# Performance work log

Hardware: AMD Instinct MI355X
Metric: run time of the kernel (lower is better)

The kernel has to match this reference:

```python
import jax, jax.numpy as jnp
import numpy as np

B, SQ, SK, DK, DV = 16, 2048, 2048, 64, 64


def setup_inputs() -> dict:
    key = jax.random.key(0)
    kq, kk, kv, km = jax.random.split(key, 4)
    Q = jax.random.normal(kq, (B, SQ, DK), dtype=jnp.float32)
    K = jax.random.normal(kk, (B, SK, DK), dtype=jnp.float32)
    V = jax.random.normal(kv, (B, SK, DV), dtype=jnp.float32)
    mask = jax.random.randint(km, (B, 1, SK), 0, 2, dtype=jnp.int32)
    return {"Q": Q, "K": K, "V": V, "mask": mask}


def reference(Q, K, V, mask):
    d = K.shape[-1]
    # scores: (B, SQ, SK) -- full attention matrix, as in the torch module
    attn = jnp.einsum("bqd,bkd->bqk", Q, K) / (d ** 0.5)
    masked = mask == 0  # (B, 1, SK), broadcasts over query dim
    attn = jnp.where(masked, jnp.float32(-1e9), attn)
    attn = jax.nn.softmax(attn, axis=-1)
    attn = jnp.where(masked, jnp.float32(0.0), attn)
    output = jnp.einsum("bqk,bkv->bqv", attn, V)
    return (output, attn)
```

## Files before the change

### kernel.cpp

```cpp
#include <hip/hip_runtime.h>

#define NB   16
#define SQL  2048
#define SKL  2048
#define DKL  64
#define DVL  64
#define NE   (NB * SQL * DKL)

typedef __attribute__((ext_vector_type(8))) short short8;
typedef __attribute__((ext_vector_type(4))) short s16x4;
typedef __attribute__((ext_vector_type(4))) float f32x4;
typedef __attribute__((ext_vector_type(4))) int   i32x4;
typedef __attribute__((ext_vector_type(4))) unsigned u32x4;

#define SCALE_LOG2E 0.1803368801111204f
#define EXP2F(x) __builtin_amdgcn_exp2f(x)
#define MFMA32(a,b,c) __builtin_amdgcn_mfma_f32_16x16x32_bf16((a),(b),(c),0,0,0)

__device__ __forceinline__ short f2bf(float x) {
    unsigned u = __builtin_bit_cast(unsigned, x);
    u = (u + 0x7fffu + ((u >> 16) & 1u)) >> 16;
    return (short)u;
}
__device__ __forceinline__ float bf2f(short s) {
    return __builtin_bit_cast(float, ((unsigned)(unsigned short)s) << 16);
}

__device__ __forceinline__ short8 pk8(f32x4 a, f32x4 b) {
    unsigned w0, w1, w2, w3;
    asm("v_cvt_pk_bf16_f32 %0, %1, %2" : "=v"(w0) : "v"(a[0]), "v"(a[1]));
    asm("v_cvt_pk_bf16_f32 %0, %1, %2" : "=v"(w1) : "v"(a[2]), "v"(a[3]));
    asm("v_cvt_pk_bf16_f32 %0, %1, %2" : "=v"(w2) : "v"(b[0]), "v"(b[1]));
    asm("v_cvt_pk_bf16_f32 %0, %1, %2" : "=v"(w3) : "v"(b[2]), "v"(b[3]));
    u32x4 t = {w0, w1, w2, w3};
    return __builtin_bit_cast(short8, t);
}

__global__ __launch_bounds__(256)
void prep(const float* __restrict__ Q, const float* __restrict__ K,
          short* __restrict__ ws)
{
    short* qhi = ws;
    short* qlo = ws + (size_t)NE;
    short* khi = ws + (size_t)2 * NE;
    short* klo = ws + (size_t)3 * NE;

    size_t i4 = ((size_t)blockIdx.x * 256 + threadIdx.x) * 4;
    if (i4 >= NE) return;

    f32x4 q = *(const f32x4*)(Q + i4);
    f32x4 k = *(const f32x4*)(K + i4);
    s16x4 qh, ql, kh, kl;
    #pragma unroll
    for (int j = 0; j < 4; j++) {
        qh[j] = f2bf(q[j]);  ql[j] = f2bf(q[j] - bf2f(qh[j]));
        kh[j] = f2bf(k[j]);  kl[j] = f2bf(k[j] - bf2f(kh[j]));
    }
    *(s16x4*)(qhi + i4) = qh;
    *(s16x4*)(qlo + i4) = ql;
    *(s16x4*)(khi + i4) = kh;
    *(s16x4*)(klo + i4) = kl;
}

__global__ __launch_bounds__(256)
void vtrans(const float* __restrict__ V, short* __restrict__ vt)
{
    __shared__ short st[64][72];
    const int b  = blockIdx.x >> 5;
    const int kt = blockIdx.x & 31;
    const int t  = threadIdx.x;

    const int kr = t >> 2;
    const int c0 = (t & 3) * 16;
    const float* vsrc = V + ((size_t)(b * SKL) + kt * 64 + kr) * DVL + c0;
    #pragma unroll
    for (int j = 0; j < 4; j++) {
        f32x4 x = *(const f32x4*)(vsrc + j * 4);
        #pragma unroll
        for (int i = 0; i < 4; i++) st[kr][c0 + j * 4 + i] = f2bf(x[i]);
    }
    __syncthreads();

    const int vr = t >> 2;
    const int cc = (t & 3) * 16;
    short* dst = vt + (size_t)b * DVL * SKL + (size_t)vr * SKL + kt * 64 + cc;
    short o[16];
    #pragma unroll
    for (int m = 0; m < 16; m++) {
        int kk = cc + m;
        int tb = kk >> 5;
        int w5 = kk & 31;
        int qd = w5 >> 3;
        int jj = w5 & 7;
        int kl = tb * 32 + qd * 4 + (jj & 3) + ((jj >> 2) << 4);
        o[m] = st[kl][vr];
    }
    *(short8*)(dst)     = *(short8*)(o);
    *(short8*)(dst + 8) = *(short8*)(o + 8);
}

__global__ __launch_bounds__(256, 4)
void attn_fwd(const short* __restrict__ ws, const int* __restrict__ mask,
              float* __restrict__ out, float* __restrict__ attn)
{
    __shared__ __align__(16) char smem[16384 + 256];
    f32x4* s_acc = (f32x4*)smem;
    float* s_red = (float*)(smem + 16384);

    const int tid  = threadIdx.x;
    const int w    = tid >> 6;
    const int lane = tid & 63;
    const int l15  = tid & 15;
    const int quad = (tid & 63) >> 4;

    const int bid = blockIdx.x;
    const int swz = (bid & 7) * ((NB * SQL / 16) >> 3) + (bid >> 3);
    const int b     = swz >> 7;
    const int qbase = (swz & 127) * 16;

    const int k0 = w * (SKL / 4);
    const int k1 = k0 + SKL / 4;

    const short* qhi = ws + (size_t)(b * SQL + qbase) * DKL;
    const short* qlo = qhi + (size_t)NE;
    const short* khi = ws + (size_t)2 * NE + (size_t)b * SKL * DKL;
    const short* klo = khi + (size_t)NE;
    const short* vtg = ws + (size_t)4 * NE + (size_t)b * DVL * SKL;
    const int*   mk  = mask + b * SKL;

    short8 qa0h = *(const short8*)(qhi + (size_t)l15 * DKL + quad * 8);
    short8 qa1h = *(const short8*)(qhi + (size_t)l15 * DKL + 32 + quad * 8);
    short8 qa0l = *(const short8*)(qlo + (size_t)l15 * DKL + quad * 8);
    short8 qa1l = *(const short8*)(qlo + (size_t)l15 * DKL + 32 + quad * 8);

    float lsum = 0.f;
    for (int kb = k0; kb < k1; kb += 32) {
        size_t o0 = (size_t)(kb + l15) * DKL + quad * 8;
        size_t o1 = o0 + (size_t)16 * DKL;
        short8 h0l = *(const short8*)(khi + o0);
        short8 h0h = *(const short8*)(khi + o0 + 32);
        short8 h1l = *(const short8*)(khi + o1);
        short8 h1h = *(const short8*)(khi + o1 + 32);
        short8 l0l = *(const short8*)(klo + o0);
        short8 l0h = *(const short8*)(klo + o0 + 32);
        short8 l1l = *(const short8*)(klo + o1);
        short8 l1h = *(const short8*)(klo + o1 + 32);
        i32x4 m0 = *(const i32x4*)(mk + kb + quad * 4);
        i32x4 m1 = *(const i32x4*)(mk + kb + 16 + quad * 4);

        f32x4 z = {0.f, 0.f, 0.f, 0.f};
        f32x4 sA0 = MFMA32(h0l, qa0h, z);
        sA0 = MFMA32(l0l, qa0h, sA0);
        sA0 = MFMA32(h0l, qa0l, sA0);
        f32x4 sB0 = MFMA32(h0h, qa1h, z);
        sB0 = MFMA32(l0h, qa1h, sB0);
        sB0 = MFMA32(h0h, qa1l, sB0);
        f32x4 sA1 = MFMA32(h1l, qa0h, z);
        sA1 = MFMA32(l1l, qa0h, sA1);
        sA1 = MFMA32(h1l, qa0l, sA1);
        f32x4 sB1 = MFMA32(h1h, qa1h, z);
        sB1 = MFMA32(l1h, qa1h, sB1);
        sB1 = MFMA32(h1h, qa1l, sB1);

        #pragma unroll
        for (int r = 0; r < 4; r++) {
            lsum += EXP2F(fmaf(sA0[r] + sB0[r], SCALE_LOG2E, m0[r] ? 0.f : -1e9f));
            lsum += EXP2F(fmaf(sA1[r] + sB1[r], SCALE_LOG2E, m1[r] ? 0.f : -1e9f));
        }
    }
    lsum += __shfl_xor(lsum, 16, 64);
    lsum += __shfl_xor(lsum, 32, 64);
    if (lane < 16) s_red[w * 16 + l15] = lsum;
    __syncthreads();
    const float tot  = s_red[l15] + s_red[16 + l15] + s_red[32 + l15] + s_red[48 + l15];
    const float lg2i = -__log2f(tot);

    f32x4 acc[4];
    #pragma unroll
    for (int vt = 0; vt < 4; vt++) { f32x4 z = {0.f,0.f,0.f,0.f}; acc[vt] = z; }

    for (int kb = k0; kb < k1; kb += 32) {
        const short* vrow = vtg + kb + quad * 8;
        short8 vv0 = *(const short8*)(vrow + (size_t)(0 * 16 + l15) * SKL);
        short8 vv1 = *(const short8*)(vrow + (size_t)(1 * 16 + l15) * SKL);
        short8 vv2 = *(const short8*)(vrow + (size_t)(2 * 16 + l15) * SKL);
        short8 vv3 = *(const short8*)(vrow + (size_t)(3 * 16 + l15) * SKL);
        i32x4 m0 = *(const i32x4*)(mk + kb + quad * 4);
        i32x4 m1 = *(const i32x4*)(mk + kb + 16 + quad * 4);

        size_t o0 = (size_t)(kb + l15) * DKL + quad * 8;
        size_t o1 = o0 + (size_t)16 * DKL;
        short8 h0l = *(const short8*)(khi + o0);
        short8 h0h = *(const short8*)(khi + o0 + 32);
        short8 h1l = *(const short8*)(khi + o1);
        short8 h1h = *(const short8*)(khi + o1 + 32);
        short8 l0l = *(const short8*)(klo + o0);
        short8 l0h = *(const short8*)(klo + o0 + 32);
        short8 l1l = *(const short8*)(klo + o1);
        short8 l1h = *(const short8*)(klo + o1 + 32);

        f32x4 z = {0.f, 0.f, 0.f, 0.f};
        f32x4 sA0 = MFMA32(h0l, qa0h, z);
        sA0 = MFMA32(l0l, qa0h, sA0);
        sA0 = MFMA32(h0l, qa0l, sA0);
        f32x4 sB0 = MFMA32(h0h, qa1h, z);
        sB0 = MFMA32(l0h, qa1h, sB0);
        sB0 = MFMA32(h0h, qa1l, sB0);
        f32x4 sA1 = MFMA32(h1l, qa0h, z);
        sA1 = MFMA32(l1l, qa0h, sA1);
        sA1 = MFMA32(h1l, qa0l, sA1);
        f32x4 sB1 = MFMA32(h1h, qa1h, z);
        sB1 = MFMA32(l1h, qa1h, sB1);
        sB1 = MFMA32(h1h, qa1l, sB1);

        f32x4 p0, p1;
        #pragma unroll
        for (int r = 0; r < 4; r++) {
            p0[r] = EXP2F(fmaf(sA0[r] + sB0[r], SCALE_LOG2E, m0[r] ? lg2i : -1e9f));
            p1[r] = EXP2F(fmaf(sA1[r] + sB1[r], SCALE_LOG2E, m1[r] ? lg2i : -1e9f));
        }

        float* arow = attn + (size_t)(b * SQL + qbase + l15) * SKL + kb + quad * 4;
        *(f32x4*)arow        = p0;
        *(f32x4*)(arow + 16) = p1;

        short8 pa = pk8(p0, p1);
        acc[0] = MFMA32(pa, vv0, acc[0]);
        acc[1] = MFMA32(pa, vv1, acc[1]);
        acc[2] = MFMA32(pa, vv2, acc[2]);
        acc[3] = MFMA32(pa, vv3, acc[3]);
    }

    #pragma unroll
    for (int vt = 0; vt < 4; vt++) s_acc[vt * 256 + w * 64 + lane] = acc[vt];
    __syncthreads();

    f32x4 t_ = s_acc[w * 256 + 0 * 64 + lane];
    #pragma unroll
    for (int wp = 1; wp < 4; wp++) {
        f32x4 u = s_acc[w * 256 + wp * 64 + lane];
        #pragma unroll
        for (int r = 0; r < 4; r++) t_[r] += u[r];
    }
    #pragma unroll
    for (int r = 0; r < 4; r++)
        out[(size_t)(b * SQL + qbase + quad * 4 + r) * DVL + w * 16 + l15] = t_[r];
}

extern "C" void kernel_launch(void* const* d_in, const int* in_sizes, int n_in,
                              void* d_out, int out_size, void* d_ws, size_t ws_size,
                              hipStream_t stream) {
    const float* Q    = (const float*)d_in[0];
    const float* K    = (const float*)d_in[1];
    const float* V    = (const float*)d_in[2];
    const int*   mask = (const int*)d_in[3];
    float* out  = (float*)d_out;
    float* attn = out + (size_t)NB * SQL * DVL;
    short* ws   = (short*)d_ws;

    prep<<<dim3(NE / (256 * 4)), dim3(256), 0, stream>>>(Q, K, ws);
    vtrans<<<dim3(NB * (SKL / 64)), dim3(256), 0, stream>>>(V, ws + (size_t)4 * NE);
    attn_fwd<<<dim3(NB * (SQL / 16)), dim3(256), 0, stream>>>(ws, mask, out, attn);
}
```

Measured before the change: 560.8 us.

## Fuse softmax passes into single pass with separate attn normalization kernel

The attention kernel now computes QK^T and exp once. It accumulates the row sum and P·V in the same loop and writes unnormalized probabilities, then divides the output by the row sum. A new kernel rescales each attention row by the reciprocal of its sum. The aim is to drop the second QK^T recompute and the extra K loads, at the cost of an extra read-modify-write of the 256MB attn matrix. It also double-buffers K/V register loads and lowers the occupancy hint to 2.

```diff
diff --git a/kernel.cpp b/kernel.cpp
--- a/kernel.cpp
+++ b/kernel.cpp
@@ -99,7 +99,61 @@
     *(short8*)(dst + 8) = *(short8*)(o + 8);
 }
 
-__global__ __launch_bounds__(256, 4)
+#define LOADK(P, kb) {                                                  \
+    size_t o0 = (size_t)((kb) + l15) * DKL + quad * 8;                  \
+    size_t o1 = o0 + (size_t)16 * DKL;                                  \
+    P##h0l = *(const short8*)(khi + o0);                                \
+    P##h0h = *(const short8*)(khi + o0 + 32);                           \
+    P##h1l = *(const short8*)(khi + o1);                                \
+    P##h1h = *(const short8*)(khi + o1 + 32);                           \
+    P##l0l = *(const short8*)(klo + o0);                                \
+    P##l0h = *(const short8*)(klo + o0 + 32);                           \
+    P##l1l = *(const short8*)(klo + o1);                                \
+    P##l1h = *(const short8*)(klo + o1 + 32);                           \
+}
+
+#define LOADV(kb) {                                                     \
+    const short* vrow = vtg + (kb) + quad * 8;                          \
+    Vv0 = *(const short8*)(vrow + (size_t)(0 * 16 + l15) * SKL);        \
+    Vv1 = *(const short8*)(vrow + (size_t)(1 * 16 + l15) * SKL);        \
+    Vv2 = *(const short8*)(vrow + (size_t)(2 * 16 + l15) * SKL);        \
+    Vv3 = *(const short8*)(vrow + (size_t)(3 * 16 + l15) * SKL);        \
+}
+
+#define STEP(P, kb) {                                                   \
+    i32x4 m0 = *(const i32x4*)(mk + (kb) + quad * 4);                   \
+    i32x4 m1 = *(const i32x4*)(mk + (kb) + 16 + quad * 4);              \
+    f32x4 z = {0.f, 0.f, 0.f, 0.f};                                     \
+    f32x4 sA0 = MFMA32(P##h0l, qa0h, z);                                \
+    sA0 = MFMA32(P##l0l, qa0h, sA0);                                    \
+    sA0 = MFMA32(P##h0l, qa0l, sA0);                                    \
+    f32x4 sB0 = MFMA32(P##h0h, qa1h, z);                                \
+    sB0 = MFMA32(P##l0h, qa1h, sB0);                                    \
+    sB0 = MFMA32(P##h0h, qa1l, sB0);                                    \
+    f32x4 sA1 = MFMA32(P##h1l, qa0h, z);                                \
+    sA1 = MFMA32(P##l1l, qa0h, sA1);                                    \
+    sA1 = MFMA32(P##h1l, qa0l, sA1);                                    \
+    f32x4 sB1 = MFMA32(P##h1h, qa1h, z);                                \
+    sB1 = MFMA32(P##l1h, qa1h, sB1);                                    \
+    sB1 = MFMA32(P##h1h, qa1l, sB1);                                    \
+    f32x4 p0, p1;                                                       \
+    _Pragma("unroll")                                                   \
+    for (int r = 0; r < 4; r++) {                                       \
+        p0[r] = EXP2F(fmaf(sA0[r] + sB0[r], SCALE_LOG2E, m0[r] ? 0.f : -1e9f)); \
+        p1[r] = EXP2F(fmaf(sA1[r] + sB1[r], SCALE_LOG2E, m1[r] ? 0.f : -1e9f)); \
+        lsum += p0[r] + p1[r];                                          \
+    }                                                                   \
+    short8 pa = pk8(p0, p1);                                            \
+    acc0 = MFMA32(pa, Vv0, acc0);                                       \
+    acc1 = MFMA32(pa, Vv1, acc1);                                       \
+    acc2 = MFMA32(pa, Vv2, acc2);                                       \
+    acc3 = MFMA32(pa, Vv3, acc3);                                       \
+    float* arow = attn + (size_t)(b * SQL + qbase + l15) * SKL + (kb) + quad * 4; \
+    *(f32x4*)arow        = p0;                                          \
+    *(f32x4*)(arow + 16) = p1;                                          \
+}
+
+__global__ __launch_bounds__(256, 2)
 void attn_fwd(const short* __restrict__ ws, const int* __restrict__ mask,
               float* __restrict__ out, float* __restrict__ attn)
 {
@@ -119,7 +173,6 @@
     const int qbase = (swz & 127) * 16;
 
     const int k0 = w * (SKL / 4);
-    const int k1 = k0 + SKL / 4;
 
     const short* qhi = ws + (size_t)(b * SQL + qbase) * DKL;
     const short* qlo = qhi + (size_t)NE;
@@ -133,106 +186,34 @@
     short8 qa0l = *(const short8*)(qlo + (size_t)l15 * DKL + quad * 8);
     short8 qa1l = *(const short8*)(qlo + (size_t)l15 * DKL + 32 + quad * 8);
 
+    f32x4 acc0 = {0.f,0.f,0.f,0.f}, acc1 = acc0, acc2 = acc0, acc3 = acc0;
     float lsum = 0.f;
-    for (int kb = k0; kb < k1; kb += 32) {
-        size_t o0 = (size_t)(kb + l15) * DKL + quad * 8;
-        size_t o1 = o0 + (size_t)16 * DKL;
-        short8 h0l = *(const short8*)(khi + o0);
-        short8 h0h = *(const short8*)(khi + o0 + 32);
-        short8 h1l = *(const short8*)(khi + o1);
-        short8 h1h = *(const short8*)(khi + o1 + 32);
-        short8 l0l = *(const short8*)(klo + o0);
-        short8 l0h = *(const short8*)(klo + o0 + 32);
-        short8 l1l = *(const short8*)(klo + o1);
-        short8 l1h = *(const short8*)(klo + o1 + 32);
-        i32x4 m0 = *(const i32x4*)(mk + kb + quad * 4);
-        i32x4 m1 = *(const i32x4*)(mk + kb + 16 + quad * 4);
-
-        f32x4 z = {0.f, 0.f, 0.f, 0.f};
-        f32x4 sA0 = MFMA32(h0l, qa0h, z);
-        sA0 = MFMA32(l0l, qa0h, sA0);
-        sA0 = MFMA32(h0l, qa0l, sA0);
-        f32x4 sB0 = MFMA32(h0h, qa1h, z);
-        sB0 = MFMA32(l0h, qa1h, sB0);
-        sB0 = MFMA32(h0h, qa1l, sB0);
-        f32x4 sA1 = MFMA32(h1l, qa0h, z);
-        sA1 = MFMA32(l1l, qa0h, sA1);
-        sA1 = MFMA32(h1l, qa0l, sA1);
-        f32x4 sB1 = MFMA32(h1h, qa1h, z);
-        sB1 = MFMA32(l1h, qa1h, sB1);
-        sB1 = MFMA32(h1h, qa1l, sB1);
-
-        #pragma unroll
-        for (int r = 0; r < 4; r++) {
-            lsum += EXP2F(fmaf(sA0[r] + sB0[r], SCALE_LOG2E, m0[r] ? 0.f : -1e9f));
-            lsum += EXP2F(fmaf(sA1[r] + sB1[r], SCALE_LOG2E, m1[r] ? 0.f : -1e9f));
-        }
-    }
+
+    short8 Ah0l, Ah0h, Ah1l, Ah1h, Al0l, Al0h, Al1l, Al1h;
+    short8 Bh0l, Bh0h, Bh1l, Bh1h, Bl0l, Bl0h, Bl1l, Bl1h;
+    short8 Vv0, Vv1, Vv2, Vv3;
+
+    LOADK(A, k0);
+    for (int it = 0; it < 8; ++it) {
+        const int kb0 = k0 + it * 64;
+        LOADV(kb0);
+        LOADK(B, kb0 + 32);
+        STEP(A, kb0);
+        LOADV(kb0 + 32);
+        const int kbn = (it < 7) ? kb0 + 64 : k0;
+        LOADK(A, kbn);
+        STEP(B, kb0 + 32);
+    }
+
     lsum += __shfl_xor(lsum, 16, 64);
     lsum += __shfl_xor(lsum, 32, 64);
     if (lane < 16) s_red[w * 16 + l15] = lsum;
     __syncthreads();
-    const float tot  = s_red[l15] + s_red[16 + l15] + s_red[32 + l15] + s_red[48 + l15];
-    const float lg2i = -__log2f(tot);
-
-    f32x4 acc[4];
-    #pragma unroll
-    for (int vt = 0; vt < 4; vt++) { f32x4 z = {0.f,0.f,0.f,0.f}; acc[vt] = z; }
-
-    for (int kb = k0; kb < k1; kb += 32) {
-        const short* vrow = vtg + kb + quad * 8;
-        short8 vv0 = *(const short8*)(vrow + (size_t)(0 * 16 + l15) * SKL);
-        short8 vv1 = *(const short8*)(vrow + (size_t)(1 * 16 + l15) * SKL);
-        short8 vv2 = *(const short8*)(vrow + (size_t)(2 * 16 + l15) * SKL);
-        short8 vv3 = *(const short8*)(vrow + (size_t)(3 * 16 + l15) * SKL);
-        i32x4 m0 = *(const i32x4*)(mk + kb + quad * 4);
-        i32x4 m1 = *(const i32x4*)(mk + kb + 16 + quad * 4);
-
-        size_t o0 = (size_t)(kb + l15) * DKL + quad * 8;
-        size_t o1 = o0 + (size_t)16 * DKL;
-        short8 h0l = *(const short8*)(khi + o0);
-        short8 h0h = *(const short8*)(khi + o0 + 32);
-        short8 h1l = *(const short8*)(khi + o1);
-        short8 h1h = *(const short8*)(khi + o1 + 32);
-        short8 l0l = *(const short8*)(klo + o0);
-        short8 l0h = *(const short8*)(klo + o0 + 32);
-        short8 l1l = *(const short8*)(klo + o1);
-        short8 l1h = *(const short8*)(klo + o1 + 32);
-
-        f32x4 z = {0.f, 0.f, 0.f, 0.f};
-        f32x4 sA0 = MFMA32(h0l, qa0h, z);
-        sA0 = MFMA32(l0l, qa0h, sA0);
-        sA0 = MFMA32(h0l, qa0l, sA0);
-        f32x4 sB0 = MFMA32(h0h, qa1h, z);
-        sB0 = MFMA32(l0h, qa1h, sB0);
-        sB0 = MFMA32(h0h, qa1l, sB0);
-        f32x4 sA1 = MFMA32(h1l, qa0h, z);
-        sA1 = MFMA32(l1l, qa0h, sA1);
-        sA1 = MFMA32(h1l, qa0l, sA1);
-        f32x4 sB1 = MFMA32(h1h, qa1h, z);
-        sB1 = MFMA32(l1h, qa1h, sB1);
-        sB1 = MFMA32(h1h, qa1l, sB1);
-
-        f32x4 p0, p1;
-        #pragma unroll
-        for (int r = 0; r < 4; r++) {
-            p0[r] = EXP2F(fmaf(sA0[r] + sB0[r], SCALE_LOG2E, m0[r] ? lg2i : -1e9f));
-            p1[r] = EXP2F(fmaf(sA1[r] + sB1[r], SCALE_LOG2E, m1[r] ? lg2i : -1e9f));
-        }
-
-        float* arow = attn + (size_t)(b * SQL + qbase + l15) * SKL + kb + quad * 4;
-        *(f32x4*)arow        = p0;
-        *(f32x4*)(arow + 16) = p1;
-
-        short8 pa = pk8(p0, p1);
-        acc[0] = MFMA32(pa, vv0, acc[0]);
-        acc[1] = MFMA32(pa, vv1, acc[1]);
-        acc[2] = MFMA32(pa, vv2, acc[2]);
-        acc[3] = MFMA32(pa, vv3, acc[3]);
-    }
-
-    #pragma unroll
-    for (int vt = 0; vt < 4; vt++) s_acc[vt * 256 + w * 64 + lane] = acc[vt];
+
+    s_acc[0 * 256 + w * 64 + lane] = acc0;
+    s_acc[1 * 256 + w * 64 + lane] = acc1;
+    s_acc[2 * 256 + w * 64 + lane] = acc2;
+    s_acc[3 * 256 + w * 64 + lane] = acc3;
     __syncthreads();
 
     f32x4 t_ = s_acc[w * 256 + 0 * 64 + lane];
@@ -243,8 +224,32 @@
         for (int r = 0; r < 4; r++) t_[r] += u[r];
     }
     #pragma unroll
-    for (int r = 0; r < 4; r++)
-        out[(size_t)(b * SQL + qbase + quad * 4 + r) * DVL + w * 16 + l15] = t_[r];
+    for (int r = 0; r < 4; r++) {
+        int rr = quad * 4 + r;
+        float tt = s_red[rr] + s_red[16 + rr] + s_red[32 + rr] + s_red[48 + rr];
+        out[(size_t)(b * SQL + qbase + rr) * DVL + w * 16 + l15] = t_[r] / tt;
+    }
+}
+
+__global__ __launch_bounds__(256)
+void norm(float* __restrict__ attn)
+{
+    __shared__ float sw[4];
+    const int row = blockIdx.x;
+    float* p = attn + (size_t)row * SKL + threadIdx.x * 8;
+    f32x4 x0 = *(const f32x4*)p;
+    f32x4 x1 = *(const f32x4*)(p + 4);
+    float s = (x0[0] + x0[1]) + (x0[2] + x0[3])
+            + (x1[0] + x1[1]) + (x1[2] + x1[3]);
+    #pragma unroll
+    for (int off = 1; off < 64; off <<= 1) s += __shfl_xor(s, off, 64);
+    if ((threadIdx.x & 63) == 0) sw[threadIdx.x >> 6] = s;
+    __syncthreads();
+    const float inv = 1.0f / ((sw[0] + sw[1]) + (sw[2] + sw[3]));
+    #pragma unroll
+    for (int r = 0; r < 4; r++) { x0[r] *= inv; x1[r] *= inv; }
+    *(f32x4*)p       = x0;
+    *(f32x4*)(p + 4) = x1;
 }
 
 extern "C" void kernel_launch(void* const* d_in, const int* in_sizes, int n_in,
@@ -261,4 +266,5 @@
     prep<<<dim3(NE / (256 * 4)), dim3(256), 0, stream>>>(Q, K, ws);
     vtrans<<<dim3(NB * (SKL / 64)), dim3(256), 0, stream>>>(V, ws + (size_t)4 * NE);
     attn_fwd<<<dim3(NB * (SQL / 16)), dim3(256), 0, stream>>>(ws, mask, out, attn);
-}
+    norm<<<dim3(NB * SQL), dim3(256), 0, stream>>>(attn);
+}
```

Measured after the change: 525.8 us. 6.2% less time.

## Replace two-pass softmax with single pass plus separate attn normalization kernel

Applied to the files above, without the earlier changes.

The attention kernel now computes QK^T once, writes unnormalized exp scores to attn, accumulates PV and row sums in the same loop, and divides the output by the row sum at the end. A new norm kernel rereads each attn row, sums it and rescales it. Each block also handles 32 query rows instead of 16 so K/V loads are shared across two row tiles. This drops the second QK^T recomputation and K reload, but adds a full extra read and write of the 256MB attn matrix and lowers occupancy. No max subtraction is used, so exp can overflow for large scores.

```diff
diff --git a/kernel.cpp b/kernel.cpp
--- a/kernel.cpp
+++ b/kernel.cpp
@@ -99,13 +99,13 @@
     *(short8*)(dst + 8) = *(short8*)(o + 8);
 }
 
-__global__ __launch_bounds__(256, 4)
+__global__ __launch_bounds__(256, 2)
 void attn_fwd(const short* __restrict__ ws, const int* __restrict__ mask,
               float* __restrict__ out, float* __restrict__ attn)
 {
-    __shared__ __align__(16) char smem[16384 + 256];
+    __shared__ __align__(16) char smem[32768 + 512];
     f32x4* s_acc = (f32x4*)smem;
-    float* s_red = (float*)(smem + 16384);
+    float* s_red = (float*)(smem + 32768);
 
     const int tid  = threadIdx.x;
     const int w    = tid >> 6;
@@ -114,12 +114,11 @@
     const int quad = (tid & 63) >> 4;
 
     const int bid = blockIdx.x;
-    const int swz = (bid & 7) * ((NB * SQL / 16) >> 3) + (bid >> 3);
-    const int b     = swz >> 7;
-    const int qbase = (swz & 127) * 16;
+    const int swz = (bid & 7) * 128 + (bid >> 3);
+    const int b     = swz >> 6;
+    const int qbase = (swz & 63) * 32;
 
     const int k0 = w * (SKL / 4);
-    const int k1 = k0 + SKL / 4;
 
     const short* qhi = ws + (size_t)(b * SQL + qbase) * DKL;
     const short* qlo = qhi + (size_t)NE;
@@ -132,9 +131,18 @@
     short8 qa1h = *(const short8*)(qhi + (size_t)l15 * DKL + 32 + quad * 8);
     short8 qa0l = *(const short8*)(qlo + (size_t)l15 * DKL + quad * 8);
     short8 qa1l = *(const short8*)(qlo + (size_t)l15 * DKL + 32 + quad * 8);
-
-    float lsum = 0.f;
-    for (int kb = k0; kb < k1; kb += 32) {
+    short8 qb0h = *(const short8*)(qhi + (size_t)(16 + l15) * DKL + quad * 8);
+    short8 qb1h = *(const short8*)(qhi + (size_t)(16 + l15) * DKL + 32 + quad * 8);
+    short8 qb0l = *(const short8*)(qlo + (size_t)(16 + l15) * DKL + quad * 8);
+    short8 qb1l = *(const short8*)(qlo + (size_t)(16 + l15) * DKL + 32 + quad * 8);
+
+    f32x4 acc00 = {0.f,0.f,0.f,0.f}, acc01 = acc00, acc02 = acc00, acc03 = acc00;
+    f32x4 acc10 = acc00, acc11 = acc00, acc12 = acc00, acc13 = acc00;
+    float lsum0 = 0.f, lsum1 = 0.f;
+
+    for (int it = 0; it < 16; ++it) {
+        const int kb = k0 + it * 32;
+
         size_t o0 = (size_t)(kb + l15) * DKL + quad * 8;
         size_t o1 = o0 + (size_t)16 * DKL;
         short8 h0l = *(const short8*)(khi + o0);
@@ -145,6 +153,11 @@
         short8 l0h = *(const short8*)(klo + o0 + 32);
         short8 l1l = *(const short8*)(klo + o1);
         short8 l1h = *(const short8*)(klo + o1 + 32);
+        const short* vrow = vtg + kb + quad * 8;
+        short8 vv0 = *(const short8*)(vrow + (size_t)(0 * 16 + l15) * SKL);
+        short8 vv1 = *(const short8*)(vrow + (size_t)(1 * 16 + l15) * SKL);
+        short8 vv2 = *(const short8*)(vrow + (size_t)(2 * 16 + l15) * SKL);
+        short8 vv3 = *(const short8*)(vrow + (size_t)(3 * 16 + l15) * SKL);
         i32x4 m0 = *(const i32x4*)(mk + kb + quad * 4);
         i32x4 m1 = *(const i32x4*)(mk + kb + 16 + quad * 4);
 
@@ -161,90 +174,112 @@
         f32x4 sB1 = MFMA32(h1h, qa1h, z);
         sB1 = MFMA32(l1h, qa1h, sB1);
         sB1 = MFMA32(h1h, qa1l, sB1);
-
+        f32x4 tA0 = MFMA32(h0l, qb0h, z);
+        tA0 = MFMA32(l0l, qb0h, tA0);
+        tA0 = MFMA32(h0l, qb0l, tA0);
+        f32x4 tB0 = MFMA32(h0h, qb1h, z);
+        tB0 = MFMA32(l0h, qb1h, tB0);
+        tB0 = MFMA32(h0h, qb1l, tB0);
+        f32x4 tA1 = MFMA32(h1l, qb0h, z);
+        tA1 = MFMA32(l1l, qb0h, tA1);
+        tA1 = MFMA32(h1l, qb0l, tA1);
+        f32x4 tB1 = MFMA32(h1h, qb1h, z);
+        tB1 = MFMA32(l1h, qb1h, tB1);
+        tB1 = MFMA32(h1h, qb1l, tB1);
+
+        f32x4 p0, p1, q0, q1;
         #pragma unroll
         for (int r = 0; r < 4; r++) {
-            lsum += EXP2F(fmaf(sA0[r] + sB0[r], SCALE_LOG2E, m0[r] ? 0.f : -1e9f));
-            lsum += EXP2F(fmaf(sA1[r] + sB1[r], SCALE_LOG2E, m1[r] ? 0.f : -1e9f));
+            float bias0 = m0[r] ? 0.f : -1e9f;
+            float bias1 = m1[r] ? 0.f : -1e9f;
+            p0[r] = EXP2F(fmaf(sA0[r] + sB0[r], SCALE_LOG2E, bias0));
+            p1[r] = EXP2F(fmaf(sA1[r] + sB1[r], SCALE_LOG2E, bias1));
+            q0[r] = EXP2F(fmaf(tA0[r] + tB0[r], SCALE_LOG2E, bias0));
+            q1[r] = EXP2F(fmaf(tA1[r] + tB1[r], SCALE_LOG2E, bias1));
+            lsum0 += p0[r] + p1[r];
+            lsum1 += q0[r] + q1[r];
         }
-    }
-    lsum += __shfl_xor(lsum, 16, 64);
-    lsum += __shfl_xor(lsum, 32, 64);
-    if (lane < 16) s_red[w * 16 + l15] = lsum;
+
+        float* a0 = attn + (size_t)(b * SQL + qbase + l15) * SKL + kb + quad * 4;
+        float* a1 = attn + (size_t)(b * SQL + qbase + 16 + l15) * SKL + kb + quad * 4;
+        *(f32x4*)a0        = p0;
+        *(f32x4*)(a0 + 16) = p1;
+        *(f32x4*)a1        = q0;
+        *(f32x4*)(a1 + 16) = q1;
+
+        short8 pa = pk8(p0, p1);
+        short8 pb = pk8(q0, q1);
+        acc00 = MFMA32(pa, vv0, acc00);
+        acc01 = MFMA32(pa, vv1, acc01);
+        acc02 = MFMA32(pa, vv2, acc02);
+        acc03 = MFMA32(pa, vv3, acc03);
+        acc10 = MFMA32(pb, vv0, acc10);
+        acc11 = MFMA32(pb, vv1, acc11);
+        acc12 = MFMA32(pb, vv2, acc12);
+        acc13 = MFMA32(pb, vv3, acc13);
+    }
+
+    lsum0 += __shfl_xor(lsum0, 16, 64);
+    lsum0 += __shfl_xor(lsum0, 32, 64);
+    lsum1 += __shfl_xor(lsum1, 16, 64);
+    lsum1 += __shfl_xor(lsum1, 32, 64);
+    if (lane < 16) {
+        s_red[w * 16 + l15]      = lsum0;
+        s_red[64 + w * 16 + l15] = lsum1;
+    }
+
+    s_acc[0 * 256 + w * 64 + lane] = acc00;
+    s_acc[1 * 256 + w * 64 + lane] = acc01;
+    s_acc[2 * 256 + w * 64 + lane] = acc02;
+    s_acc[3 * 256 + w * 64 + lane] = acc03;
+    s_acc[4 * 256 + w * 64 + lane] = acc10;
+    s_acc[5 * 256 + w * 64 + lane] = acc11;
+    s_acc[6 * 256 + w * 64 + lane] = acc12;
+    s_acc[7 * 256 + w * 64 + lane] = acc13;
     __syncthreads();
-    const float tot  = s_red[l15] + s_red[16 + l15] + s_red[32 + l15] + s_red[48 + l15];
-    const float lg2i = -__log2f(tot);
-
-    f32x4 acc[4];
-    #pragma unroll
-    for (int vt = 0; vt < 4; vt++) { f32x4 z = {0.f,0.f,0.f,0.f}; acc[vt] = z; }
-
-    for (int kb = k0; kb < k1; kb += 32) {
-        const short* vrow = vtg + kb + quad * 8;
-        short8 vv0 = *(const short8*)(vrow + (size_t)(0 * 16 + l15) * SKL);
-        short8 vv1 = *(const short8*)(vrow + (size_t)(1 * 16 + l15) * SKL);
-        short8 vv2 = *(const short8*)(vrow + (size_t)(2 * 16 + l15) * SKL);
-        short8 vv3 = *(const short8*)(vrow + (size_t)(3 * 16 + l15) * SKL);
-        i32x4 m0 = *(const i32x4*)(mk + kb + quad * 4);
-        i32x4 m1 = *(const i32x4*)(mk + kb + 16 + quad * 4);
-
-        size_t o0 = (size_t)(kb + l15) * DKL + quad * 8;
-        size_t o1 = o0 + (size_t)16 * DKL;
-        short8 h0l = *(const short8*)(khi + o0);
-        short8 h0h = *(const short8*)(khi + o0 + 32);
-        short8 h1l = *(const short8*)(khi + o1);
-        short8 h1h = *(const short8*)(khi + o1 + 32);
-        short8 l0l = *(const short8*)(klo + o0);
-        short8 l0h = *(const short8*)(klo + o0 + 32);
-        short8 l1l = *(const short8*)(klo + o1);
-        short8 l1h = *(const short8*)(klo + o1 + 32);
-
-        f32x4 z = {0.f, 0.f, 0.f, 0.f};
-        f32x4 sA0 = MFMA32(h0l, qa0h, z);
-        sA0 = MFMA32(l0l, qa0h, sA0);
-        sA0 = MFMA32(h0l, qa0l, sA0);
-        f32x4 sB0 = MFMA32(h0h, qa1h, z);
-        sB0 = MFMA32(l0h, qa1h, sB0);
-        sB0 = MFMA32(h0h, qa1l, sB0);
-        f32x4 sA1 = MFMA32(h1l, qa0h, z);
-        sA1 = MFMA32(l1l, qa0h, sA1);
-        sA1 = MFMA32(h1l, qa0l, sA1);
-        f32x4 sB1 = MFMA32(h1h, qa1h, z);
-        sB1 = MFMA32(l1h, qa1h, sB1);
-        sB1 = MFMA32(h1h, qa1l, sB1);
-
-        f32x4 p0, p1;
+
+    #pragma unroll
+    for (int c = 0; c < 2; c++) {
+        const int T  = w * 2 + c;
+        const int g  = T >> 2;
+        const int vt = T & 3;
+        f32x4 t_ = s_acc[T * 256 + 0 * 64 + lane];
+        #pragma unroll
+        for (int wp = 1; wp < 4; wp++) {
+            f32x4 u = s_acc[T * 256 + wp * 64 + lane];
+            #pragma unroll
+            for (int r = 0; r < 4; r++) t_[r] += u[r];
+        }
         #pragma unroll
         for (int r = 0; r < 4; r++) {
-            p0[r] = EXP2F(fmaf(sA0[r] + sB0[r], SCALE_LOG2E, m0[r] ? lg2i : -1e9f));
-            p1[r] = EXP2F(fmaf(sA1[r] + sB1[r], SCALE_LOG2E, m1[r] ? lg2i : -1e9f));
+            const int qr = quad * 4 + r;
+            float tt = s_red[g * 64 + qr]      + s_red[g * 64 + 16 + qr]
+                     + s_red[g * 64 + 32 + qr] + s_red[g * 64 + 48 + qr];
+            out[(size_t)(b * SQL + qbase + g * 16 + qr) * DVL + vt * 16 + l15] =
+                t_[r] / tt;
         }
-
-        float* arow = attn + (size_t)(b * SQL + qbase + l15) * SKL + kb + quad * 4;
-        *(f32x4*)arow        = p0;
-        *(f32x4*)(arow + 16) = p1;
-
-        short8 pa = pk8(p0, p1);
-        acc[0] = MFMA32(pa, vv0, acc[0]);
-        acc[1] = MFMA32(pa, vv1, acc[1]);
-        acc[2] = MFMA32(pa, vv2, acc[2]);
-        acc[3] = MFMA32(pa, vv3, acc[3]);
-    }
-
-    #pragma unroll
-    for (int vt = 0; vt < 4; vt++) s_acc[vt * 256 + w * 64 + lane] = acc[vt];
+    }
+}
+
+__global__ __launch_bounds__(256)
+void norm(float* __restrict__ attn)
+{
+    __shared__ float sw[4];
+    const int row = blockIdx.x;
+    float* p = attn + (size_t)row * SKL + threadIdx.x * 8;
+    f32x4 x0 = *(const f32x4*)p;
+    f32x4 x1 = *(const f32x4*)(p + 4);
+    float s = (x0[0] + x0[1]) + (x0[2] + x0[3])
+            + (x1[0] + x1[1]) + (x1[2] + x1[3]);
+    #pragma unroll
+    for (int off = 1; off < 64; off <<= 1) s += __shfl_xor(s, off, 64);
+    if ((threadIdx.x & 63) == 0) sw[threadIdx.x >> 6] = s;
     __syncthreads();
-
-    f32x4 t_ = s_acc[w * 256 + 0 * 64 + lane];
-    #pragma unroll
-    for (int wp = 1; wp < 4; wp++) {
-        f32x4 u = s_acc[w * 256 + wp * 64 + lane];
-        #pragma unroll
-        for (int r = 0; r < 4; r++) t_[r] += u[r];
-    }
-    #pragma unroll
-    for (int r = 0; r < 4; r++)
-        out[(size_t)(b * SQL + qbase + quad * 4 + r) * DVL + w * 16 + l15] = t_[r];
+    const float inv = 1.0f / ((sw[0] + sw[1]) + (sw[2] + sw[3]));
+    #pragma unroll
+    for (int r = 0; r < 4; r++) { x0[r] *= inv; x1[r] *= inv; }
+    *(f32x4*)p       = x0;
+    *(f32x4*)(p + 4) = x1;
 }
 
 extern "C" void kernel_launch(void* const* d_in, const int* in_sizes, int n_in,
@@ -260,5 +295,6 @@
 
     prep<<<dim3(NE / (256 * 4)), dim3(256), 0, stream>>>(Q, K, ws);
     vtrans<<<dim3(NB * (SKL / 64)), dim3(256), 0, stream>>>(V, ws + (size_t)4 * NE);
-    attn_fwd<<<dim3(NB * (SQL / 16)), dim3(256), 0, stream>>>(ws, mask, out, attn);
-}
+    attn_fwd<<<dim3(NB * (SQL / 32)), dim3(256), 0, stream>>>(ws, mask, out, attn);
+    norm<<<dim3(NB * SQL), dim3(256), 0, stream>>>(attn);
+}
```

Result: faster. 448.8 us (-20.0%).
